# Optimization experiments

Measured on AMD Instinct MI355X. Metric: run time of the kernel, lower is better.

The kernel has to match this reference:

```python
import jax, jax.numpy as jnp
import numpy as np

N = 200000
E = 12800000
G = 1024

def setup_inputs() -> dict:
    key = jax.random.key(0)
    k1, k2, k3 = jax.random.split(key, 3)
    node_pos = jax.random.normal(k1, (N, 2), dtype=jnp.float32)
    edge_index = jax.random.randint(k2, (2, E), 0, N, dtype=jnp.int64)
    batch_ids = jnp.sort(jax.random.randint(k3, (N,), 0, G, dtype=jnp.int64))
    return {"node_pos": node_pos, "edge_index": edge_index,
            "batch_ids": batch_ids, "num_graphs": G}

def reference(node_pos, edge_index, batch_ids, num_graphs):
    # gather edge endpoints: [E, 2]
    start = node_pos[edge_index[0]]
    end = node_pos[edge_index[1]]
    # per-edge loss: (||end - start|| - 1)^2, [E]
    diff = end - start
    eu = jnp.sqrt(jnp.sum(diff * diff, axis=1))
    edge_var = jnp.square(eu - 1.0)
    # scatter-mean by graph id of the edge's source node
    seg = batch_ids[edge_index[0]]
    sums = jax.ops.segment_sum(edge_var, seg, num_segments=num_graphs)
    counts = jax.ops.segment_sum(jnp.ones_like(edge_var), seg, num_segments=num_graphs)
    graph_var = sums / jnp.maximum(counts, 1.0)  # [G]
    # self.reduce = torch.mean over graphs
    return jnp.mean(graph_var)
```

## Files before the change

### kernel.cpp

```cpp
#include <hip/hip_runtime.h>


typedef int iv4 __attribute__((ext_vector_type(4)));
typedef unsigned int u32;

#define GBINS 1024

__device__ __forceinline__ int find_graph(int v, const int* __restrict__ ss, float scale) {
    int g = (int)((float)v * scale);
    g = min(g, GBINS - 1);
    while (v < ss[g]) --g;
    while (v >= ss[g + 1]) ++g;
    return g;
}

__global__ void prep(const int* __restrict__ batch, int* __restrict__ startg,
                     float* __restrict__ gsum, u32* __restrict__ gcnt, int N) {
    const int i = blockIdx.x * blockDim.x + threadIdx.x;
    if (i < GBINS) { gsum[i] = 0.f; gcnt[i] = 0u; }
    if (i >= N) return;
    const int b = batch[i];
    if (i == 0) { for (int g = 0; g <= b; ++g) startg[g] = 0; }
    else { const int a = batch[i - 1]; for (int g = a + 1; g <= b; ++g) startg[g] = i; }
    if (i == N - 1) { for (int g = b + 1; g <= GBINS; ++g) startg[g] = N; }
}

__global__ __launch_bounds__(512)
void fused_kernel(const int* __restrict__ src, const int* __restrict__ dst,
                  const float2* __restrict__ pos, const int* __restrict__ startg,
                  float* __restrict__ gsum, u32* __restrict__ gcnt,
                  int E, float scale) {
    __shared__ int ss[GBINS + 1];
    __shared__ float hs[GBINS];
    __shared__ u32 hc[GBINS];
    const int tid = threadIdx.x;
    for (int i = tid; i < GBINS + 1; i += 512) ss[i] = startg[i];
    for (int i = tid; i < GBINS; i += 512) { hs[i] = 0.f; hc[i] = 0u; }
    __syncthreads();

    const int ngroups = E >> 2;
    const iv4* __restrict__ s4 = (const iv4*)src;
    const iv4* __restrict__ d4 = (const iv4*)dst;
    const int gtid = blockIdx.x * 512 + tid, gstride = gridDim.x * 512;

    for (int i = gtid; i < ngroups; i += gstride) {
        const iv4 sv = __builtin_nontemporal_load(&s4[i]);
        const iv4 dv = __builtin_nontemporal_load(&d4[i]);
        float2 pa[4], pb[4];
        #pragma unroll
        for (int k = 0; k < 4; ++k) { pa[k] = pos[sv[k]]; pb[k] = pos[dv[k]]; }
        #pragma unroll
        for (int k = 0; k < 4; ++k) {
            const float dx = pb[k].x - pa[k].x;
            const float dy = pb[k].y - pa[k].y;
            const float t  = sqrtf(fmaf(dx, dx, dy * dy)) - 1.f;
            const int g = find_graph(sv[k], ss, scale);
            atomicAdd(&hs[g], t * t);
            atomicAdd(&hc[g], 1u);
        }
    }
    for (int e = (ngroups << 2) + gtid; e < E; e += gstride) {
        const int s = src[e], d = dst[e];
        const float2 a = pos[s], b = pos[d];
        const float dx = b.x - a.x, dy = b.y - a.y;
        const float t  = sqrtf(fmaf(dx, dx, dy * dy)) - 1.f;
        const int g = find_graph(s, ss, scale);
        atomicAdd(&hs[g], t * t);
        atomicAdd(&hc[g], 1u);
    }

    __syncthreads();
    for (int j = tid; j < GBINS; j += 512) {
        const int g = (j + (blockIdx.x << 3)) & (GBINS - 1);
        const u32 c = hc[g];
        if (c) { atomicAdd(&gcnt[g], c); atomicAdd(&gsum[g], hs[g]); }
    }
}

__global__ void finalize_kernel(const float* __restrict__ gsum,
                                const u32* __restrict__ gcnt,
                                float* __restrict__ out,
                                const int* __restrict__ nG_ptr) {
    const int G = *nG_ptr;
    float v = 0.f;
    for (int g = threadIdx.x; g < G; g += blockDim.x)
        v += gsum[g] / fmaxf((float)gcnt[g], 1.f);
    __shared__ float w[16];
    for (int off = 32; off; off >>= 1) v += __shfl_down(v, off, 64);
    if ((threadIdx.x & 63) == 0) w[threadIdx.x >> 6] = v;
    __syncthreads();
    if (threadIdx.x == 0) {
        float s = 0.f;
        const int nw = (blockDim.x + 63) >> 6;
        for (int i = 0; i < nw; ++i) s += w[i];
        out[0] = s / (float)G;
    }
}

extern "C" void kernel_launch(void* const* d_in, const int* in_sizes, int n_in,
                              void* d_out, int out_size, void* d_ws, size_t ws_size,
                              hipStream_t stream) {
    const float2* pos   = (const float2*)d_in[0];
    const int*    ei    = (const int*)d_in[1];
    const int*    batch = (const int*)d_in[2];
    const int*    nG    = (const int*)d_in[3];

    const int N = in_sizes[0] / 2;
    const int E = in_sizes[1] / 2;
    const int* src = ei;
    const int* dst = ei + E;

    float* gsum   = (float*)d_ws;
    u32*   gcnt   = (u32*)((char*)d_ws + 4096);
    int*   startg = (int*)((char*)d_ws + 8192);

    const float scale = (float)GBINS / (float)N;
    prep<<<(N + 255) / 256, 256, 0, stream>>>(batch, startg, gsum, gcnt, N);
    fused_kernel<<<625, 512, 0, stream>>>(src, dst, pos, startg, gsum, gcnt, E, scale);
    finalize_kernel<<<1, 1024, 0, stream>>>(gsum, gcnt, (float*)d_out, nG);
}
```

Before: 271.0 us.

## Replace grid-stride edge loop with dynamic per-wave chunk work stealing

Swaps the static grid-stride loop over edge groups for dynamic scheduling. Each wavefront grabs 64-group chunks from one of 8 global atomic counters, each counter covering one partition of the edge range. The grid also grows from 625 to 1024 blocks. The aim is to balance load across CUs and waves where random gathers and LDS atomics make latency uneven, at the cost of extra global atomics and a shuffle per chunk, plus partitioned rather than interleaved memory access.

Measured after the change: 307.9 us. +13.6%, slower.

```diff
diff --git a/kernel.cpp b/kernel.cpp
--- a/kernel.cpp
+++ b/kernel.cpp
@@ -5,6 +5,9 @@
 typedef unsigned int u32;
 
 #define GBINS 1024
+#define NCTR  8
+#define CTRSTRIDE 16
+#define CHUNK 64
 
 __device__ __forceinline__ int find_graph(int v, const int* __restrict__ ss, float scale) {
     int g = (int)((float)v * scale);
@@ -15,9 +18,11 @@
 }
 
 __global__ void prep(const int* __restrict__ batch, int* __restrict__ startg,
-                     float* __restrict__ gsum, u32* __restrict__ gcnt, int N) {
+                     float* __restrict__ gsum, u32* __restrict__ gcnt,
+                     u32* __restrict__ ctr, int N) {
     const int i = blockIdx.x * blockDim.x + threadIdx.x;
     if (i < GBINS) { gsum[i] = 0.f; gcnt[i] = 0u; }
+    if (i < NCTR * CTRSTRIDE) ctr[i] = 0u;
     if (i >= N) return;
     const int b = batch[i];
     if (i == 0) { for (int g = 0; g <= b; ++g) startg[g] = 0; }
@@ -29,7 +34,7 @@
 void fused_kernel(const int* __restrict__ src, const int* __restrict__ dst,
                   const float2* __restrict__ pos, const int* __restrict__ startg,
                   float* __restrict__ gsum, u32* __restrict__ gcnt,
-                  int E, float scale) {
+                  u32* __restrict__ ctr, int E, float scale) {
     __shared__ int ss[GBINS + 1];
     __shared__ float hs[GBINS];
     __shared__ u32 hc[GBINS];
@@ -41,24 +46,43 @@
     const int ngroups = E >> 2;
     const iv4* __restrict__ s4 = (const iv4*)src;
     const iv4* __restrict__ d4 = (const iv4*)dst;
+
+    const int c   = blockIdx.x & (NCTR - 1);
+    const int per = (ngroups + NCTR - 1) / NCTR;
+    const int lo  = c * per;
+    const int rn  = min(per, ngroups - lo);
+    const int lane = tid & 63;
+    u32* __restrict__ myctr = &ctr[c * CTRSTRIDE];
+
+    int cur = 0;
+    if (lane == 0) cur = (int)atomicAdd(myctr, (u32)CHUNK);
+    cur = __shfl(cur, 0, 64);
+
+    while (cur < rn) {
+        int nxt = 0;
+        if (lane == 0) nxt = (int)atomicAdd(myctr, (u32)CHUNK);
+        const int g_idx = cur + lane;
+        if (g_idx < rn) {
+            const int gi = lo + g_idx;
+            const iv4 sv = __builtin_nontemporal_load(&s4[gi]);
+            const iv4 dv = __builtin_nontemporal_load(&d4[gi]);
+            float2 pa[4], pb[4];
+            #pragma unroll
+            for (int k = 0; k < 4; ++k) { pa[k] = pos[sv[k]]; pb[k] = pos[dv[k]]; }
+            #pragma unroll
+            for (int k = 0; k < 4; ++k) {
+                const float dx = pb[k].x - pa[k].x;
+                const float dy = pb[k].y - pa[k].y;
+                const float t  = sqrtf(fmaf(dx, dx, dy * dy)) - 1.f;
+                const int g = find_graph(sv[k], ss, scale);
+                atomicAdd(&hs[g], t * t);
+                atomicAdd(&hc[g], 1u);
+            }
+        }
+        cur = __shfl(nxt, 0, 64);
+    }
+
     const int gtid = blockIdx.x * 512 + tid, gstride = gridDim.x * 512;
-
-    for (int i = gtid; i < ngroups; i += gstride) {
-        const iv4 sv = __builtin_nontemporal_load(&s4[i]);
-        const iv4 dv = __builtin_nontemporal_load(&d4[i]);
-        float2 pa[4], pb[4];
-        #pragma unroll
-        for (int k = 0; k < 4; ++k) { pa[k] = pos[sv[k]]; pb[k] = pos[dv[k]]; }
-        #pragma unroll
-        for (int k = 0; k < 4; ++k) {
-            const float dx = pb[k].x - pa[k].x;
-            const float dy = pb[k].y - pa[k].y;
-            const float t  = sqrtf(fmaf(dx, dx, dy * dy)) - 1.f;
-            const int g = find_graph(sv[k], ss, scale);
-            atomicAdd(&hs[g], t * t);
-            atomicAdd(&hc[g], 1u);
-        }
-    }
     for (int e = (ngroups << 2) + gtid; e < E; e += gstride) {
         const int s = src[e], d = dst[e];
         const float2 a = pos[s], b = pos[d];
@@ -72,8 +96,8 @@
     __syncthreads();
     for (int j = tid; j < GBINS; j += 512) {
         const int g = (j + (blockIdx.x << 3)) & (GBINS - 1);
-        const u32 c = hc[g];
-        if (c) { atomicAdd(&gcnt[g], c); atomicAdd(&gsum[g], hs[g]); }
+        const u32 cc = hc[g];
+        if (cc) { atomicAdd(&gcnt[g], cc); atomicAdd(&gsum[g], hs[g]); }
     }
 }
 
@@ -113,9 +137,10 @@
     float* gsum   = (float*)d_ws;
     u32*   gcnt   = (u32*)((char*)d_ws + 4096);
     int*   startg = (int*)((char*)d_ws + 8192);
+    u32*   ctr    = (u32*)((char*)d_ws + 12800);
 
     const float scale = (float)GBINS / (float)N;
-    prep<<<(N + 255) / 256, 256, 0, stream>>>(batch, startg, gsum, gcnt, N);
-    fused_kernel<<<625, 512, 0, stream>>>(src, dst, pos, startg, gsum, gcnt, E, scale);
+    prep<<<(N + 255) / 256, 256, 0, stream>>>(batch, startg, gsum, gcnt, ctr, N);
+    fused_kernel<<<1024, 512, 0, stream>>>(src, dst, pos, startg, gsum, gcnt, ctr, E, scale);
     finalize_kernel<<<1, 1024, 0, stream>>>(gsum, gcnt, (float*)d_out, nG);
 }
```

## Fuse finalize into main kernel via last-block-done counter, raise grid size

Applied to the files above, without the earlier changes.

Removes the separate finalize launch: each block increments a global done counter after flushing its histogram, and the last block reads the global sums and counts atomically and computes the mean. The grid also grows from 625 to 1024 blocks. This saves one kernel launch and its tail gap, at the cost of a threadfence and atomic per block and more per-block histogram init and flush traffic from the larger grid.

After: 510.3 us. 1.88x slower.

```diff
diff --git a/kernel.cpp b/kernel.cpp
--- a/kernel.cpp
+++ b/kernel.cpp
@@ -15,8 +15,10 @@
 }
 
 __global__ void prep(const int* __restrict__ batch, int* __restrict__ startg,
-                     float* __restrict__ gsum, u32* __restrict__ gcnt, int N) {
+                     float* __restrict__ gsum, u32* __restrict__ gcnt,
+                     u32* __restrict__ done, int N) {
     const int i = blockIdx.x * blockDim.x + threadIdx.x;
+    if (i == 0) *done = 0u;
     if (i < GBINS) { gsum[i] = 0.f; gcnt[i] = 0u; }
     if (i >= N) return;
     const int b = batch[i];
@@ -29,7 +31,8 @@
 void fused_kernel(const int* __restrict__ src, const int* __restrict__ dst,
                   const float2* __restrict__ pos, const int* __restrict__ startg,
                   float* __restrict__ gsum, u32* __restrict__ gcnt,
-                  int E, float scale) {
+                  u32* __restrict__ done, float* __restrict__ out,
+                  const int* __restrict__ nG_ptr, int E, float scale) {
     __shared__ int ss[GBINS + 1];
     __shared__ float hs[GBINS];
     __shared__ u32 hc[GBINS];
@@ -75,25 +78,29 @@
         const u32 c = hc[g];
         if (c) { atomicAdd(&gcnt[g], c); atomicAdd(&gsum[g], hs[g]); }
     }
-}
 
-__global__ void finalize_kernel(const float* __restrict__ gsum,
-                                const u32* __restrict__ gcnt,
-                                float* __restrict__ out,
-                                const int* __restrict__ nG_ptr) {
-    const int G = *nG_ptr;
-    float v = 0.f;
-    for (int g = threadIdx.x; g < G; g += blockDim.x)
-        v += gsum[g] / fmaxf((float)gcnt[g], 1.f);
-    __shared__ float w[16];
-    for (int off = 32; off; off >>= 1) v += __shfl_down(v, off, 64);
-    if ((threadIdx.x & 63) == 0) w[threadIdx.x >> 6] = v;
+    __threadfence();
+    __shared__ u32 amlast;
+    if (tid == 0) amlast = (atomicAdd(done, 1u) == (u32)(gridDim.x - 1)) ? 1u : 0u;
     __syncthreads();
-    if (threadIdx.x == 0) {
-        float s = 0.f;
-        const int nw = (blockDim.x + 63) >> 6;
-        for (int i = 0; i < nw; ++i) s += w[i];
-        out[0] = s / (float)G;
+    if (amlast) {
+        const int G = *nG_ptr;
+        float v = 0.f;
+        for (int g = tid; g < G; g += 512) {
+            const float s = atomicAdd(&gsum[g], 0.f);
+            const u32   c = atomicAdd(&gcnt[g], 0u);
+            v += s / fmaxf((float)c, 1.f);
+        }
+        __shared__ float w[8];
+        for (int off = 32; off; off >>= 1) v += __shfl_down(v, off, 64);
+        if ((tid & 63) == 0) w[tid >> 6] = v;
+        __syncthreads();
+        if (tid == 0) {
+            float s = 0.f;
+            #pragma unroll
+            for (int i2 = 0; i2 < 8; ++i2) s += w[i2];
+            out[0] = s / (float)G;
+        }
     }
 }
 
@@ -113,9 +120,10 @@
     float* gsum   = (float*)d_ws;
     u32*   gcnt   = (u32*)((char*)d_ws + 4096);
     int*   startg = (int*)((char*)d_ws + 8192);
+    u32*   done   = (u32*)((char*)d_ws + 12800);
 
     const float scale = (float)GBINS / (float)N;
-    prep<<<(N + 255) / 256, 256, 0, stream>>>(batch, startg, gsum, gcnt, N);
-    fused_kernel<<<625, 512, 0, stream>>>(src, dst, pos, startg, gsum, gcnt, E, scale);
-    finalize_kernel<<<1, 1024, 0, stream>>>(gsum, gcnt, (float*)d_out, nG);
+    prep<<<(N + 255) / 256, 256, 0, stream>>>(batch, startg, gsum, gcnt, done, N);
+    fused_kernel<<<1024, 512, 0, stream>>>(src, dst, pos, startg, gsum, gcnt,
+                                           done, (float*)d_out, nG, E, scale);
 }
```
